# Performance work log

Hardware: AMD Instinct MI355X
Metric: run time of the kernel (lower is better)

Reference implementation:

```python
import jax, jax.numpy as jnp
import numpy as np

N = 1536          # num_nodes
NODE_DIM = 128
EDGE_DIM = 32
HIDDEN = 64
THRESHOLD = 0.5   # forward() default


def setup_inputs() -> dict:
    key = jax.random.key(0)
    ks = jax.random.split(key, 13)
    s = 0.05
    f32 = jnp.float32
    return {
        "node_features": jax.random.normal(ks[0], (N, NODE_DIM), f32),
        # node_encoder: Linear(node_dim,H) -> ReLU -> Linear(H,H)
        "W1": jax.random.normal(ks[1], (HIDDEN, NODE_DIM), f32) * s,
        "b1": jax.random.normal(ks[2], (HIDDEN,), f32) * s,
        "W2": jax.random.normal(ks[3], (HIDDEN, HIDDEN), f32) * s,
        "b2": jax.random.normal(ks[4], (HIDDEN,), f32) * s,
        # edge_predictor: Linear(2H,H) -> ReLU -> Linear(H,1)
        "Wp1": jax.random.normal(ks[5], (HIDDEN, 2 * HIDDEN), f32) * s,
        "bp1": jax.random.normal(ks[6], (HIDDEN,), f32) * s,
        "wp2": jax.random.normal(ks[7], (1, HIDDEN), f32) * s,
        "bp2": jax.random.normal(ks[8], (1,), f32) * s,
        # edge_feature_predictor: Linear(2H,H) -> ReLU -> Linear(H,edge_dim)
        "Wf1": jax.random.normal(ks[9], (HIDDEN, 2 * HIDDEN), f32) * s,
        "bf1": jax.random.normal(ks[10], (HIDDEN,), f32) * s,
        "Wf2": jax.random.normal(ks[11], (EDGE_DIM, HIDDEN), f32) * s,
        "bf2": jax.random.normal(ks[12], (EDGE_DIM,), f32) * s,
    }


def reference(node_features, W1, b1, W2, b2, Wp1, bp1, wp2, bp2, Wf1, bf1, Wf2, bf2):
    # node_encoder
    enc = jax.nn.relu(node_features @ W1.T + b1) @ W2.T + b2  # [N, H]

    # all unordered pairs i < j (static shapes)
    iu_np, ju_np = np.triu_indices(N, 1)  # each [P], P = N(N-1)/2
    iu = jnp.asarray(iu_np, jnp.int32)
    ju = jnp.asarray(ju_np, jnp.int32)

    # concat([e_i, e_j]) @ W.T == e_i @ W[:, :H].T + e_j @ W[:, H:].T
    Ap = enc @ Wp1[:, :HIDDEN].T  # [N, H]
    Bp = enc @ Wp1[:, HIDDEN:].T  # [N, H]
    logits = jax.nn.relu(Ap[iu] + Bp[ju] + bp1) @ wp2[0] + bp2[0]  # [P]
    mask = jax.nn.sigmoid(logits) > THRESHOLD  # [P] bool

    Af = enc @ Wf1[:, :HIDDEN].T
    Bf = enc @ Wf1[:, HIDDEN:].T
    feat = jax.nn.relu(Af[iu] + Bf[ju] + bf1) @ Wf2.T + bf2  # [P, edge_dim]
    feat = jnp.where(mask[:, None], feat, jnp.zeros((), feat.dtype))

    # original emits [[i, j], [j, i]] per accepted pair; we emit all pairs
    # interleaved with a validity mask (padded / masked form, jit-friendly)
    row0 = jnp.stack([iu, ju], axis=1).reshape(-1)  # [2P] sources
    row1 = jnp.stack([ju, iu], axis=1).reshape(-1)  # [2P] targets
    edge_index = jnp.stack([row0, row1])            # [2, 2P]
    edge_attr = jnp.repeat(feat, 2, axis=0)         # [2P, edge_dim]
    edge_mask = jnp.repeat(mask, 2)                 # [2P] bool
    return (edge_index, edge_mask, edge_attr)
```

## Files before the change

kernel.cpp:

```cpp
#include <hip/hip_runtime.h>
#include <hip/hip_bf16.h>

#define N_NODES 1536
#define PP 1178880LL

typedef __attribute__((ext_vector_type(8))) short short8v;
typedef __attribute__((ext_vector_type(4))) float f32x4;


static __device__ __forceinline__ unsigned pack_bf16(float a, float b) {
    union { __hip_bfloat162 h; unsigned u; } cv;
    cv.h = __float22bfloat162_rn(make_float2(a, b));
    return cv.u;
}

__global__ __launch_bounds__(64) void k1_encode(
    const float* __restrict__ X,  const float* __restrict__ W1, const float* __restrict__ b1,
    const float* __restrict__ W2, const float* __restrict__ b2,
    const float* __restrict__ Wp1, const float* __restrict__ bp1,
    const float* __restrict__ Wf1, const float* __restrict__ bf1,
    double* __restrict__ Ap_d, double* __restrict__ BpT_d,
    float* __restrict__ Apf, float* __restrict__ BpTf,
    float* __restrict__ Af_f, float* __restrict__ Bf_f)
{
    const int i = blockIdx.x;
    const int t = threadIdx.x;
    __shared__ double sh1[64];
    __shared__ double se[64];

    double acc = (double)b1[t];
    const float4* Xv  = (const float4*)(X  + (size_t)i * 128);
    const float4* W1v = (const float4*)(W1 + (size_t)t * 128);
    #pragma unroll
    for (int d = 0; d < 32; ++d) {
        float4 x = Xv[d]; float4 w = W1v[d];
        acc += (double)x.x * (double)w.x + (double)x.y * (double)w.y
             + (double)x.z * (double)w.z + (double)x.w * (double)w.w;
    }
    sh1[t] = acc > 0.0 ? acc : 0.0;
    __syncthreads();

    double e = (double)b2[t];
    const float4* W2v = (const float4*)(W2 + (size_t)t * 64);
    #pragma unroll
    for (int d = 0; d < 16; ++d) {
        float4 w = W2v[d];
        e += sh1[d*4+0] * (double)w.x + sh1[d*4+1] * (double)w.y
           + sh1[d*4+2] * (double)w.z + sh1[d*4+3] * (double)w.w;
    }
    __syncthreads();
    se[t] = e;
    __syncthreads();

    double ap = (double)bp1[t], bp = 0.0, af = (double)bf1[t], bf = 0.0;
    const float4* WpA = (const float4*)(Wp1 + (size_t)t * 128);
    const float4* WpB = (const float4*)(Wp1 + (size_t)t * 128 + 64);
    const float4* WfA = (const float4*)(Wf1 + (size_t)t * 128);
    const float4* WfB = (const float4*)(Wf1 + (size_t)t * 128 + 64);
    #pragma unroll
    for (int d = 0; d < 16; ++d) {
        double e0 = se[d*4+0], e1 = se[d*4+1], e2 = se[d*4+2], e3 = se[d*4+3];
        float4 wa = WpA[d], wb = WpB[d], fa = WfA[d], fb = WfB[d];
        ap += e0*(double)wa.x + e1*(double)wa.y + e2*(double)wa.z + e3*(double)wa.w;
        bp += e0*(double)wb.x + e1*(double)wb.y + e2*(double)wb.z + e3*(double)wb.w;
        af += e0*(double)fa.x + e1*(double)fa.y + e2*(double)fa.z + e3*(double)fa.w;
        bf += e0*(double)fb.x + e1*(double)fb.y + e2*(double)fb.z + e3*(double)fb.w;
    }
    Ap_d[(size_t)i * 64 + t]       = ap;
    BpT_d[(size_t)t * N_NODES + i] = bp;
    Apf[(size_t)i * 64 + t]        = (float)ap;
    BpTf[(size_t)t * N_NODES + i]  = (float)bp;
    Af_f[(size_t)i * 64 + t]       = (float)af;
    Bf_f[(size_t)i * 64 + t]       = (float)bf;
}

__global__ __launch_bounds__(256, 4) void k2_pairs(
    const double* __restrict__ Ap_d, const double* __restrict__ BpT_d,
    const float* __restrict__ Apf, const float* __restrict__ BpTf,
    const float* __restrict__ Af_f, const float* __restrict__ Bf_f,
    const float* __restrict__ wp2, const float* __restrict__ bp2,
    const float* __restrict__ Wf2, const float* __restrict__ bf2,
    float* __restrict__ out)
{
    const int bj = blockIdx.x, bi = blockIdx.y;
    const int i0 = bi * 16, j0 = bj * 64;
    if (i0 >= j0 + 63) return;

    __shared__ float sBp[64 * 64];
    __shared__ float sBf[64 * 64];
    __shared__ float sAf[16 * 64];
    const int tid = threadIdx.x;

    {
        float4* sBp4w = (float4*)sBp;
        const float4* gBp4 = (const float4*)BpTf;
        #pragma unroll
        for (int a = 0; a < 4; ++a) {
            int F = tid + a * 256;
            int k = F >> 4, q = F & 15;
            sBp4w[F] = gBp4[(size_t)k * (N_NODES / 4) + (j0 >> 2) + q];
        }
        float4* sBf4w = (float4*)sBf;
        const float4* gBf4 = (const float4*)Bf_f;
        #pragma unroll
        for (int a = 0; a < 4; ++a) {
            int F = tid + a * 256;
            int jr = F >> 4, s = F & 15;
            sBf4w[jr * 16 + (s ^ (jr & 7))] = gBf4[(size_t)(j0 + jr) * 16 + s];
        }
        float4* sAf4w = (float4*)sAf;
        const float4* gAf4 = (const float4*)Af_f;
        sAf4w[tid] = gAf4[(size_t)(i0 + (tid >> 4)) * 16 + (tid & 15)];
    }

    const int w = tid >> 6, lane = tid & 63;
    const int lr = lane & 15, hi = lane >> 4;

    short8v wfrag[2][2];
    #pragma unroll
    for (int cb = 0; cb < 2; ++cb) {
        #pragma unroll
        for (int kb = 0; kb < 2; ++kb) {
            const float4* src = (const float4*)(Wf2 + (size_t)(cb * 16 + lr) * 64 + kb * 32 + hi * 8);
            float4 s0 = src[0], s1 = src[1];
            union { short8v s; uint4 u; } cv;
            cv.u.x = pack_bf16(s0.x, s0.y);
            cv.u.y = pack_bf16(s0.z, s0.w);
            cv.u.z = pack_bf16(s1.x, s1.y);
            cv.u.w = pack_bf16(s1.z, s1.w);
            wfrag[cb][kb] = cv.s;
        }
    }

    __syncthreads();

    const int j = j0 + lane;
    const float  bp2f = bp2[0];
    const double bp2v = (double)bp2[0];
    const float4* sBf4 = (const float4*)sBf;
    const float4* sAf4 = (const float4*)sAf;

    for (int ii = 0; ii < 4; ++ii) {
        const int i = i0 + w * 4 + ii;
        if (i >= j0 + 63) break;
        const int il = i - i0;

        const float* aprowf = Apf + (size_t)i * 64;
        float logf = bp2f;
        #pragma unroll
        for (int k = 0; k < 64; ++k) {
            float hb = aprowf[k] + sBp[k * 64 + lane];
            hb = hb > 0.f ? hb : 0.f;
            logf = fmaf(hb, wp2[k], logf);
        }
        bool maskb = logf > 0.f;
        if (__any(fabsf(logf) < 4e-6f)) {
            const double* aprow = Ap_d + (size_t)i * 64;
            double logit = bp2v;
            for (int k = 0; k < 64; ++k) {
                double hb = aprow[k] + BpT_d[(size_t)k * N_NODES + j];
                hb = hb > 0.0 ? hb : 0.0;
                logit = fma(hb, (double)wp2[k], logit);
            }
            maskb = logit > 0.0;
        }
        const unsigned long long bal = __ballot(maskb);

        f32x4 acc[2][4];
        #pragma unroll
        for (int cb = 0; cb < 2; ++cb)
            #pragma unroll
            for (int jb = 0; jb < 4; ++jb) {
                f32x4 z; z[0] = 0.f; z[1] = 0.f; z[2] = 0.f; z[3] = 0.f;
                acc[cb][jb] = z;
            }

        #pragma unroll
        for (int jb = 0; jb < 4; ++jb) {
            const int jl = jb * 16 + lr;
            #pragma unroll
            for (int kb = 0; kb < 2; ++kb) {
                float4 a0 = sAf4[il * 16 + kb * 8 + hi * 2 + 0];
                float4 a1 = sAf4[il * 16 + kb * 8 + hi * 2 + 1];
                float4 b0 = sBf4[jl * 16 + ((kb * 8 + hi * 2 + 0) ^ (jl & 7))];
                float4 b1 = sBf4[jl * 16 + ((kb * 8 + hi * 2 + 1) ^ (jl & 7))];
                float r0 = fmaxf(a0.x + b0.x, 0.f), r1 = fmaxf(a0.y + b0.y, 0.f);
                float r2 = fmaxf(a0.z + b0.z, 0.f), r3 = fmaxf(a0.w + b0.w, 0.f);
                float r4 = fmaxf(a1.x + b1.x, 0.f), r5 = fmaxf(a1.y + b1.y, 0.f);
                float r6 = fmaxf(a1.z + b1.z, 0.f), r7 = fmaxf(a1.w + b1.w, 0.f);
                union { short8v s; uint4 u; } cv;
                cv.u.x = pack_bf16(r0, r1);
                cv.u.y = pack_bf16(r2, r3);
                cv.u.z = pack_bf16(r4, r5);
                cv.u.w = pack_bf16(r6, r7);
                acc[0][jb] = __builtin_amdgcn_mfma_f32_16x16x32_bf16(wfrag[0][kb], cv.s, acc[0][jb], 0, 0, 0);
                acc[1][jb] = __builtin_amdgcn_mfma_f32_16x16x32_bf16(wfrag[1][kb], cv.s, acc[1][jb], 0, 0, 0);
            }
        }

        if (j > i) {
            const float m = ((bal >> lane) & 1ull) ? 1.0f : 0.0f;
            const long long p = (long long)i * (N_NODES - 1)
                              - ((long long)i * (i - 1)) / 2 + (j - i - 1);
            ((float2*)out)[p]            = make_float2((float)i, (float)j);
            ((float2*)(out + 2 * PP))[p] = make_float2((float)j, (float)i);
            ((float2*)(out + 4 * PP))[p] = make_float2(m, m);
        }
        float4 bof0 = *(const float4*)(bf2 + 0 * 16 + hi * 4);
        float4 bof1 = *(const float4*)(bf2 + 1 * 16 + hi * 4);
        #pragma unroll
        for (int jb = 0; jb < 4; ++jb) {
            const int jf = j0 + jb * 16 + lr;
            if (jf > i) {
                const float mv = ((bal >> (jb * 16 + lr)) & 1ull) ? 1.0f : 0.0f;
                const long long p = (long long)i * (N_NODES - 1)
                                  - ((long long)i * (i - 1)) / 2 + (jf - i - 1);
                float* ab = out + 6 * PP + (p << 6) + hi * 4;
                float4 v0 = make_float4((acc[0][jb][0] + bof0.x) * mv,
                                        (acc[0][jb][1] + bof0.y) * mv,
                                        (acc[0][jb][2] + bof0.z) * mv,
                                        (acc[0][jb][3] + bof0.w) * mv);
                float4 v1 = make_float4((acc[1][jb][0] + bof1.x) * mv,
                                        (acc[1][jb][1] + bof1.y) * mv,
                                        (acc[1][jb][2] + bof1.z) * mv,
                                        (acc[1][jb][3] + bof1.w) * mv);
                *(float4*)(ab + 0)       = v0;
                *(float4*)(ab + 16)      = v1;
                *(float4*)(ab + 32)      = v0;
                *(float4*)(ab + 48)      = v1;
            }
        }
    }
}

extern "C" void kernel_launch(void* const* d_in, const int* in_sizes, int n_in,
                              void* d_out, int out_size, void* d_ws, size_t ws_size,
                              hipStream_t stream) {
    const float* X   = (const float*)d_in[0];
    const float* W1  = (const float*)d_in[1];
    const float* b1  = (const float*)d_in[2];
    const float* W2  = (const float*)d_in[3];
    const float* b2  = (const float*)d_in[4];
    const float* Wp1 = (const float*)d_in[5];
    const float* bp1 = (const float*)d_in[6];
    const float* wp2 = (const float*)d_in[7];
    const float* bp2 = (const float*)d_in[8];
    const float* Wf1 = (const float*)d_in[9];
    const float* bf1 = (const float*)d_in[10];
    const float* Wf2 = (const float*)d_in[11];
    const float* bf2 = (const float*)d_in[12];

    char* ws = (char*)d_ws;
    double* Ap_d  = (double*)(ws + 0);
    double* BpT_d = (double*)(ws + 786432);
    float*  Apf   = (float*)(ws + 1572864);
    float*  BpTf  = (float*)(ws + 1966080);
    float*  Af_f  = (float*)(ws + 2359296);
    float*  Bf_f  = (float*)(ws + 2752512);
    float*  out   = (float*)d_out;

    hipLaunchKernelGGL(k1_encode, dim3(N_NODES), dim3(64), 0, stream,
                       X, W1, b1, W2, b2, Wp1, bp1, Wf1, bf1,
                       Ap_d, BpT_d, Apf, BpTf, Af_f, Bf_f);

    hipLaunchKernelGGL(k2_pairs, dim3(24, 96), dim3(256), 0, stream,
                       Ap_d, BpT_d, Apf, BpTf, Af_f, Bf_f, wp2, bp2, Wf2, bf2, out);
}
```

Baseline: 122.5 us.

## Split pair kernel into logit and attribute kernels with compact triangular grid

Splits the fused pair kernel into two launches. The first computes logits, masks and the index/mask outputs and stores per-row 64-bit ballot masks in workspace. The second reads those masks and runs the MFMA attribute computation and stores. Both use a compact 1D grid over only upper-triangular tiles, replacing the 2D grid whose lower-triangle blocks exited early, and the logit loop is vectorized with float4 loads of Apf and wp2. The aim is lower register and LDS pressure per kernel and no idle blocks, at the cost of an extra launch and a round trip of the mask through global memory.

```diff
diff --git a/kernel.cpp b/kernel.cpp
--- a/kernel.cpp
+++ b/kernel.cpp
@@ -3,6 +3,7 @@
 
 #define N_NODES 1536
 #define PP 1178880LL
+#define NJB 24
 
 typedef __attribute__((ext_vector_type(8))) short short8v;
 typedef __attribute__((ext_vector_type(4))) float f32x4;
@@ -12,6 +13,14 @@
     union { __hip_bfloat162 h; unsigned u; } cv;
     cv.h = __float22bfloat162_rn(make_float2(a, b));
     return cv.u;
+}
+
+static __device__ __forceinline__ void decode_tile(int t, int& bi, int& bj) {
+    int b = (int)((sqrtf(2.0f * (float)t + 1.0f) - 1.0f) * 0.5f);
+    while (2 * b * (b + 1) > t) --b;
+    while (2 * (b + 1) * (b + 2) <= t) ++b;
+    bj = b;
+    bi = t - 2 * b * (b + 1);
 }
 
 __global__ __launch_bounds__(64) void k1_encode(
@@ -74,84 +83,53 @@
     Bf_f[(size_t)i * 64 + t]       = (float)bf;
 }
 
-__global__ __launch_bounds__(256, 4) void k2_pairs(
+__global__ __launch_bounds__(256) void k2_logit(
     const double* __restrict__ Ap_d, const double* __restrict__ BpT_d,
     const float* __restrict__ Apf, const float* __restrict__ BpTf,
-    const float* __restrict__ Af_f, const float* __restrict__ Bf_f,
     const float* __restrict__ wp2, const float* __restrict__ bp2,
-    const float* __restrict__ Wf2, const float* __restrict__ bf2,
-    float* __restrict__ out)
+    float* __restrict__ out, unsigned long long* __restrict__ maskw)
 {
-    const int bj = blockIdx.x, bi = blockIdx.y;
+    int bi, bj; decode_tile(blockIdx.x, bi, bj);
     const int i0 = bi * 16, j0 = bj * 64;
-    if (i0 >= j0 + 63) return;
 
     __shared__ float sBp[64 * 64];
-    __shared__ float sBf[64 * 64];
-    __shared__ float sAf[16 * 64];
     const int tid = threadIdx.x;
-
     {
-        float4* sBp4w = (float4*)sBp;
-        const float4* gBp4 = (const float4*)BpTf;
+        float4* s4 = (float4*)sBp;
+        const float4* g4 = (const float4*)BpTf;
         #pragma unroll
         for (int a = 0; a < 4; ++a) {
             int F = tid + a * 256;
             int k = F >> 4, q = F & 15;
-            sBp4w[F] = gBp4[(size_t)k * (N_NODES / 4) + (j0 >> 2) + q];
-        }
-        float4* sBf4w = (float4*)sBf;
-        const float4* gBf4 = (const float4*)Bf_f;
-        #pragma unroll
-        for (int a = 0; a < 4; ++a) {
-            int F = tid + a * 256;
-            int jr = F >> 4, s = F & 15;
-            sBf4w[jr * 16 + (s ^ (jr & 7))] = gBf4[(size_t)(j0 + jr) * 16 + s];
-        }
-        float4* sAf4w = (float4*)sAf;
-        const float4* gAf4 = (const float4*)Af_f;
-        sAf4w[tid] = gAf4[(size_t)(i0 + (tid >> 4)) * 16 + (tid & 15)];
-    }
+            s4[F] = g4[(size_t)k * (N_NODES / 4) + (j0 >> 2) + q];
+        }
+    }
+    __syncthreads();
 
     const int w = tid >> 6, lane = tid & 63;
-    const int lr = lane & 15, hi = lane >> 4;
-
-    short8v wfrag[2][2];
-    #pragma unroll
-    for (int cb = 0; cb < 2; ++cb) {
-        #pragma unroll
-        for (int kb = 0; kb < 2; ++kb) {
-            const float4* src = (const float4*)(Wf2 + (size_t)(cb * 16 + lr) * 64 + kb * 32 + hi * 8);
-            float4 s0 = src[0], s1 = src[1];
-            union { short8v s; uint4 u; } cv;
-            cv.u.x = pack_bf16(s0.x, s0.y);
-            cv.u.y = pack_bf16(s0.z, s0.w);
-            cv.u.z = pack_bf16(s1.x, s1.y);
-            cv.u.w = pack_bf16(s1.z, s1.w);
-            wfrag[cb][kb] = cv.s;
-        }
-    }
-
-    __syncthreads();
-
     const int j = j0 + lane;
     const float  bp2f = bp2[0];
     const double bp2v = (double)bp2[0];
-    const float4* sBf4 = (const float4*)sBf;
-    const float4* sAf4 = (const float4*)sAf;
 
     for (int ii = 0; ii < 4; ++ii) {
         const int i = i0 + w * 4 + ii;
         if (i >= j0 + 63) break;
-        const int il = i - i0;
-
-        const float* aprowf = Apf + (size_t)i * 64;
+
+        const float4* av = (const float4*)(Apf + (size_t)i * 64);
+        const float4* wv = (const float4*)wp2;
         float logf = bp2f;
         #pragma unroll
-        for (int k = 0; k < 64; ++k) {
-            float hb = aprowf[k] + sBp[k * 64 + lane];
-            hb = hb > 0.f ? hb : 0.f;
-            logf = fmaf(hb, wp2[k], logf);
+        for (int k4 = 0; k4 < 16; ++k4) {
+            float4 a = av[k4], wk = wv[k4];
+            const float* bb = sBp + k4 * 256 + lane;
+            float h0 = fmaxf(a.x + bb[0],   0.f);
+            float h1 = fmaxf(a.y + bb[64],  0.f);
+            float h2 = fmaxf(a.z + bb[128], 0.f);
+            float h3 = fmaxf(a.w + bb[192], 0.f);
+            logf = fmaf(h0, wk.x, logf);
+            logf = fmaf(h1, wk.y, logf);
+            logf = fmaf(h2, wk.z, logf);
+            logf = fmaf(h3, wk.w, logf);
         }
         bool maskb = logf > 0.f;
         if (__any(fabsf(logf) < 4e-6f)) {
@@ -165,6 +143,77 @@
             maskb = logit > 0.0;
         }
         const unsigned long long bal = __ballot(maskb);
+        if (lane == 0) maskw[(size_t)i * NJB + bj] = bal;
+
+        if (j > i) {
+            const float m = ((bal >> lane) & 1ull) ? 1.0f : 0.0f;
+            const long long p = (long long)i * (N_NODES - 1)
+                              - ((long long)i * (i - 1)) / 2 + (j - i - 1);
+            ((float2*)out)[p]            = make_float2((float)i, (float)j);
+            ((float2*)(out + 2 * PP))[p] = make_float2((float)j, (float)i);
+            ((float2*)(out + 4 * PP))[p] = make_float2(m, m);
+        }
+    }
+}
+
+__global__ __launch_bounds__(256) void k2_attr(
+    const float* __restrict__ Af_f, const float* __restrict__ Bf_f,
+    const float* __restrict__ Wf2, const float* __restrict__ bf2,
+    const unsigned long long* __restrict__ maskw,
+    float* __restrict__ out)
+{
+    int bi, bj; decode_tile(blockIdx.x, bi, bj);
+    const int i0 = bi * 16, j0 = bj * 64;
+
+    __shared__ float sBf[64 * 64];
+    __shared__ float sAf[16 * 64];
+    const int tid = threadIdx.x;
+    {
+        float4* sBf4w = (float4*)sBf;
+        const float4* gBf4 = (const float4*)Bf_f;
+        #pragma unroll
+        for (int a = 0; a < 4; ++a) {
+            int F = tid + a * 256;
+            int jr = F >> 4, s = F & 15;
+            sBf4w[jr * 16 + (s ^ (jr & 7))] = gBf4[(size_t)(j0 + jr) * 16 + s];
+        }
+        float4* sAf4w = (float4*)sAf;
+        const float4* gAf4 = (const float4*)Af_f;
+        sAf4w[tid] = gAf4[(size_t)(i0 + (tid >> 4)) * 16 + (tid & 15)];
+    }
+
+    const int w = tid >> 6, lane = tid & 63;
+    const int lr = lane & 15, hi = lane >> 4;
+
+    short8v wfrag[2][2];
+    #pragma unroll
+    for (int cb = 0; cb < 2; ++cb) {
+        #pragma unroll
+        for (int kb = 0; kb < 2; ++kb) {
+            const float4* src = (const float4*)(Wf2 + (size_t)(cb * 16 + lr) * 64 + kb * 32 + hi * 8);
+            float4 s0 = src[0], s1 = src[1];
+            union { short8v s; uint4 u; } cv;
+            cv.u.x = pack_bf16(s0.x, s0.y);
+            cv.u.y = pack_bf16(s0.z, s0.w);
+            cv.u.z = pack_bf16(s1.x, s1.y);
+            cv.u.w = pack_bf16(s1.z, s1.w);
+            wfrag[cb][kb] = cv.s;
+        }
+    }
+
+    __syncthreads();
+
+    const float4* sBf4 = (const float4*)sBf;
+    const float4* sAf4 = (const float4*)sAf;
+    const float4 bof0 = *(const float4*)(bf2 + 0 * 16 + hi * 4);
+    const float4 bof1 = *(const float4*)(bf2 + 1 * 16 + hi * 4);
+
+    for (int ii = 0; ii < 4; ++ii) {
+        const int i = i0 + w * 4 + ii;
+        if (i >= j0 + 63) break;
+        const int il = i - i0;
+
+        const unsigned long long bal = maskw[(size_t)i * NJB + bj];
 
         f32x4 acc[2][4];
         #pragma unroll
@@ -198,16 +247,6 @@
             }
         }
 
-        if (j > i) {
-            const float m = ((bal >> lane) & 1ull) ? 1.0f : 0.0f;
-            const long long p = (long long)i * (N_NODES - 1)
-                              - ((long long)i * (i - 1)) / 2 + (j - i - 1);
-            ((float2*)out)[p]            = make_float2((float)i, (float)j);
-            ((float2*)(out + 2 * PP))[p] = make_float2((float)j, (float)i);
-            ((float2*)(out + 4 * PP))[p] = make_float2(m, m);
-        }
-        float4 bof0 = *(const float4*)(bf2 + 0 * 16 + hi * 4);
-        float4 bof1 = *(const float4*)(bf2 + 1 * 16 + hi * 4);
         #pragma unroll
         for (int jb = 0; jb < 4; ++jb) {
             const int jf = j0 + jb * 16 + lr;
@@ -224,10 +263,10 @@
                                         (acc[1][jb][1] + bof1.y) * mv,
                                         (acc[1][jb][2] + bof1.z) * mv,
                                         (acc[1][jb][3] + bof1.w) * mv);
-                *(float4*)(ab + 0)       = v0;
-                *(float4*)(ab + 16)      = v1;
-                *(float4*)(ab + 32)      = v0;
-                *(float4*)(ab + 48)      = v1;
+                *(float4*)(ab + 0)  = v0;
+                *(float4*)(ab + 16) = v1;
+                *(float4*)(ab + 32) = v0;
+                *(float4*)(ab + 48) = v1;
             }
         }
     }
@@ -257,12 +296,16 @@
     float*  BpTf  = (float*)(ws + 1966080);
     float*  Af_f  = (float*)(ws + 2359296);
     float*  Bf_f  = (float*)(ws + 2752512);
+    unsigned long long* maskw = (unsigned long long*)(ws + 3145728);
     float*  out   = (float*)d_out;
 
     hipLaunchKernelGGL(k1_encode, dim3(N_NODES), dim3(64), 0, stream,
                        X, W1, b1, W2, b2, Wp1, bp1, Wf1, bf1,
                        Ap_d, BpT_d, Apf, BpTf, Af_f, Bf_f);
 
-    hipLaunchKernelGGL(k2_pairs, dim3(24, 96), dim3(256), 0, stream,
-                       Ap_d, BpT_d, Apf, BpTf, Af_f, Bf_f, wp2, bp2, Wf2, bf2, out);
-}
+    hipLaunchKernelGGL(k2_logit, dim3(1200), dim3(256), 0, stream,
+                       Ap_d, BpT_d, Apf, BpTf, wp2, bp2, out, maskw);
+
+    hipLaunchKernelGGL(k2_attr, dim3(1200), dim3(256), 0, stream,
+                       Af_f, Bf_f, Wf2, bf2, maskw, out);
+}
```

Measured after the change: 121.4 us. Within noise of the previous version (-0.9%).
